# Optimization experiments

Hardware: AMD Instinct MI355X
Metric: run time of the kernel (lower is better)

Reference implementation:

```python
import jax, jax.numpy as jnp
import numpy as np

DIM = 2048
NUM_HEADS = 16
HEAD_DIM = DIM // NUM_HEADS
FF_MULT = 2
ROPE_BASE = 10000.0
EPS = 1e-6


def _rmsnorm(x, g):
    return x * jax.lax.rsqrt(jnp.mean(x * x, axis=-1, keepdims=True) + EPS) * g


def _rope_tables(seq_len):
    half = HEAD_DIM // 2
    inv_freq = 1.0 / (ROPE_BASE ** (2.0 * jnp.arange(half, dtype=jnp.float32) / HEAD_DIM))
    angles = jnp.arange(seq_len, dtype=jnp.float32)[:, None] * inv_freq[None, :]  # (S, half)
    return jnp.cos(angles), jnp.sin(angles)


def _apply_rope(x, cos, sin):
    # x: (B, H, S, D); cos/sin: (S, D/2). Interleaved pairs (RoFormer form).
    x_even = x[..., 0::2]
    x_odd = x[..., 1::2]
    c = cos[None, None].astype(x.dtype)
    s = sin[None, None].astype(x.dtype)
    rot_even = x_even * c - x_odd * s
    rot_odd = x_odd * c + x_even * s
    return jnp.stack([rot_even, rot_odd], axis=-1).reshape(x.shape)


def setup_inputs() -> dict:
    key = jax.random.key(0)
    ks = jax.random.split(key, 7)
    B, S = 2, 2048
    scale = 1.0 / np.sqrt(DIM)
    return {
        "x": jax.random.normal(ks[0], (B, S, DIM), dtype=jnp.float32),
        "w_qkv": jax.random.normal(ks[1], (DIM, 3 * DIM), dtype=jnp.float32) * scale,
        "w_out": jax.random.normal(ks[2], (DIM, DIM), dtype=jnp.float32) * scale,
        "w_fc": jax.random.normal(ks[3], (DIM, DIM * FF_MULT), dtype=jnp.float32) * scale,
        "w_proj": jax.random.normal(ks[4], (DIM * FF_MULT, DIM), dtype=jnp.float32) / np.sqrt(DIM * FF_MULT),
        "g_in": jnp.ones((DIM,), dtype=jnp.float32),
        "g_ff": jnp.ones((DIM,), dtype=jnp.float32),
    }


def reference(x, w_qkv, w_out, w_fc, w_proj, g_in, g_ff):
    B, S, D = x.shape
    # --- attention branch ---
    h = _rmsnorm(x, g_in)
    qkv = h @ w_qkv  # (B, S, 3D)
    q, k, v = jnp.split(qkv, 3, axis=-1)
    def heads(t):
        return t.reshape(B, S, NUM_HEADS, HEAD_DIM).transpose(0, 2, 1, 3)
    q, k, v = heads(q), heads(k), heads(v)  # (B, H, S, Dh)
    cos, sin = _rope_tables(S)
    q = _apply_rope(q, cos, sin)
    k = _apply_rope(k, cos, sin)
    scores = jnp.einsum("bhqd,bhkd->bhqk", q, k) / jnp.asarray(np.sqrt(HEAD_DIM), x.dtype)
    causal = jnp.tril(jnp.ones((S, S), dtype=bool))
    scores = jnp.where(causal[None, None], scores, jnp.asarray(-jnp.inf, scores.dtype))
    attn = jax.nn.softmax(scores, axis=-1)
    out = jnp.einsum("bhqk,bhkd->bhqd", attn, v)  # (B, H, S, Dh)
    out = out.transpose(0, 2, 1, 3).reshape(B, S, D)
    x = x + out @ w_out
    # --- feed-forward branch ---
    h = _rmsnorm(x, g_ff)
    x = x + jax.nn.gelu(h @ w_fc) @ w_proj
    return x


if __name__ == "__main__":
    inp = setup_inputs()
    y = reference(**inp)
    print(y.shape, y.dtype)
```

## Files before the change

kernel.cpp:

```cpp
#include <hip/hip_runtime.h>
#include <math.h>

typedef __bf16 bf16x8 __attribute__((ext_vector_type(8)));
typedef float  f32x4  __attribute__((ext_vector_type(4)));

#define DEV __device__ __forceinline__

DEV void gload16(const void* g, void* l) {
  __builtin_amdgcn_global_load_lds(
      (const __attribute__((address_space(1))) void*)g,
      (__attribute__((address_space(3))) void*)l, 16, 0, 0);
}

__global__ __launch_bounds__(256) void transpose_cvt(
    const float* __restrict__ in, __bf16* __restrict__ outT, int R, int C) {
  __shared__ float t[64][65];
  const int c0 = blockIdx.x * 64, r0 = blockIdx.y * 64;
  const int tid = threadIdx.x;
#pragma unroll
  for (int i = 0; i < 4; i++) {
    int r = (tid >> 4) + i * 16;
    int cf = tid & 15;
    float4 v = *(const float4*)(in + (size_t)(r0 + r) * C + c0 + cf * 4);
    t[r][cf * 4 + 0] = v.x; t[r][cf * 4 + 1] = v.y;
    t[r][cf * 4 + 2] = v.z; t[r][cf * 4 + 3] = v.w;
  }
  __syncthreads();
#pragma unroll
  for (int i = 0; i < 2; i++) {
    int c = (tid >> 3) + i * 32;
    int r8 = tid & 7;
    bf16x8 ov;
#pragma unroll
    for (int k = 0; k < 8; k++) ov[k] = (__bf16)t[r8 * 8 + k][c];
    *(bf16x8*)(outT + (size_t)(c0 + c) * R + r0 + r8 * 8) = ov;
  }
}

__global__ __launch_bounds__(256) void rmsnorm_kernel(
    const float* __restrict__ x, const float* __restrict__ g, __bf16* __restrict__ out) {
  const int r = blockIdx.x, t = threadIdx.x;
  const float4* xr = (const float4*)(x + (size_t)r * 2048);
  float4 a = xr[2 * t], b = xr[2 * t + 1];
  float ss = a.x * a.x + a.y * a.y + a.z * a.z + a.w * a.w +
             b.x * b.x + b.y * b.y + b.z * b.z + b.w * b.w;
#pragma unroll
  for (int mk = 1; mk < 64; mk <<= 1) ss += __shfl_xor(ss, mk);
  __shared__ float red[4];
  if ((t & 63) == 0) red[t >> 6] = ss;
  __syncthreads();
  const float sc = rsqrtf((red[0] + red[1] + red[2] + red[3]) * (1.0f / 2048.0f) + 1e-6f);
  const float4* gr = (const float4*)g;
  float4 ga = gr[2 * t], gb = gr[2 * t + 1];
  bf16x8 ov;
  ov[0] = (__bf16)(a.x * sc * ga.x); ov[1] = (__bf16)(a.y * sc * ga.y);
  ov[2] = (__bf16)(a.z * sc * ga.z); ov[3] = (__bf16)(a.w * sc * ga.w);
  ov[4] = (__bf16)(b.x * sc * gb.x); ov[5] = (__bf16)(b.y * sc * gb.y);
  ov[6] = (__bf16)(b.z * sc * gb.z); ov[7] = (__bf16)(b.w * sc * gb.w);
  *(bf16x8*)(out + (size_t)r * 2048 + t * 8) = ov;
}

template <int EPI>
__global__ __launch_bounds__(256) void gemm_bt(
    const __bf16* __restrict__ A, const __bf16* __restrict__ BT,
    void* __restrict__ Cout, const float* __restrict__ res, int M, int N, int K) {
  __shared__ char lds[32768];
  char* As = lds;
  char* Bs = lds + 16384;
  const int tid = threadIdx.x;
  const int lane = tid & 63;
  const int bn = blockIdx.x, bm = blockIdx.y;
  const int wm = tid >> 7, wn = (tid >> 6) & 1;

  f32x4 acc[4][4];
#pragma unroll
  for (int i = 0; i < 4; i++)
#pragma unroll
    for (int j = 0; j < 4; j++) acc[i][j] = (f32x4){0.f, 0.f, 0.f, 0.f};

  const size_t strideA = (size_t)K * 2;
  const char* ga[4];
  const char* gb[4];
#pragma unroll
  for (int t = 0; t < 4; t++) {
    int gg = t * 256 + tid;
    int row = gg >> 3, slot = gg & 7;
    ga[t] = (const char*)A + (size_t)(bm * 128 + row) * strideA + ((slot ^ (row & 7)) << 4);
    gb[t] = (const char*)BT + (size_t)(bn * 128 + row) * strideA + ((slot ^ (row & 7)) << 4);
  }

  for (int k0 = 0; k0 < K; k0 += 64) {
    __syncthreads();
#pragma unroll
    for (int t = 0; t < 4; t++) {
      int gg = t * 256 + tid;
      gload16(ga[t], As + gg * 16);
      gload16(gb[t], Bs + gg * 16);
      ga[t] += 128;
      gb[t] += 128;
    }
    __syncthreads();
#pragma unroll
    for (int kk = 0; kk < 2; kk++) {
      bf16x8 a[4], b[4];
      const int c16 = kk * 4 + (lane >> 4);
#pragma unroll
      for (int i = 0; i < 4; i++) {
        int ra = wm * 64 + i * 16 + (lane & 15);
        a[i] = *(const bf16x8*)(As + ra * 128 + ((c16 ^ (ra & 7)) << 4));
        int rb = wn * 64 + i * 16 + (lane & 15);
        b[i] = *(const bf16x8*)(Bs + rb * 128 + ((c16 ^ (rb & 7)) << 4));
      }
#pragma unroll
      for (int i = 0; i < 4; i++)
#pragma unroll
        for (int j = 0; j < 4; j++)
          acc[i][j] = __builtin_amdgcn_mfma_f32_16x16x32_bf16(a[i], b[j], acc[i][j], 0, 0, 0);
    }
  }

#pragma unroll
  for (int i = 0; i < 4; i++)
#pragma unroll
    for (int j = 0; j < 4; j++)
#pragma unroll
      for (int r = 0; r < 4; r++) {
        int row = bm * 128 + wm * 64 + i * 16 + ((lane >> 4) << 2) + r;
        int col = bn * 128 + wn * 64 + j * 16 + (lane & 15);
        size_t idx = (size_t)row * N + col;
        float v = acc[i][j][r];
        if (EPI == 0) {
          ((__bf16*)Cout)[idx] = (__bf16)v;
        } else if (EPI == 1) {
          ((float*)Cout)[idx] = v + res[idx];
        } else {
          float u = 0.7978845608028654f * (v + 0.044715f * v * v * v);
          ((__bf16*)Cout)[idx] = (__bf16)(0.5f * v * (1.0f + tanhf(u)));
        }
      }
}

#define MMQ(IB, JB, AR, BR)                                                   \
  __builtin_amdgcn_s_setprio(1);                                              \
  _Pragma("unroll") for (int i = 0; i < 4; i++)                               \
      _Pragma("unroll") for (int j = 0; j < 2; j++)                           \
          _Pragma("unroll") for (int kk = 0; kk < 2; kk++)                    \
              acc[(IB)*4 + i][(JB)*2 + j] =                                   \
      __builtin_amdgcn_mfma_f32_16x16x32_bf16(                                \
          AR[i][kk], BR[j][kk], acc[(IB)*4 + i][(JB)*2 + j], 0, 0, 0);        \
  __builtin_amdgcn_s_setprio(0);

template <int EPI>
__global__ __launch_bounds__(512, 2) void gemm256(
    const __bf16* __restrict__ A, const __bf16* __restrict__ BT,
    void* __restrict__ Cout, const float* __restrict__ res, int M, int N, int K) {
  __shared__ char lds[131072];
  const int tid = threadIdx.x, lane = tid & 63, w = tid >> 6;
  const int wm = w >> 2, wn = w & 3;
  const int bn = blockIdx.x, bm = blockIdx.y;

  f32x4 acc[8][4];
#pragma unroll
  for (int i = 0; i < 8; i++)
#pragma unroll
    for (int j = 0; j < 4; j++) acc[i][j] = (f32x4){0.f, 0.f, 0.f, 0.f};

  const size_t strideA = (size_t)K * 2;
  const int r0 = tid >> 3, s0 = tid & 7;
  const int r1 = r0 + 64;
  const char* Ab0 = (const char*)A + (size_t)(bm * 256) * strideA;
  const char* Bb0 = (const char*)BT + (size_t)(bn * 256) * strideA;

  auto stage = [&](int isB, int h, int kt, int buf) {
    const char* g = (isB ? Bb0 : Ab0) + (size_t)(h * 128) * strideA + (size_t)kt * 128;
    char* d = lds + isB * 65536 + buf * 32768 + h * 16384;
    gload16(g + (size_t)r0 * strideA + ((s0 ^ (r0 & 7)) << 4), d + tid * 16);
    gload16(g + (size_t)r1 * strideA + ((s0 ^ (r1 & 7)) << 4), d + (tid + 512) * 16);
  };
  auto ldA = [&](bf16x8 (&a)[4][2], int buf, int bank) {
    const char* base = lds + buf * 32768 + wm * 16384;
#pragma unroll
    for (int i = 0; i < 4; i++)
#pragma unroll
      for (int kk = 0; kk < 2; kk++) {
        int rl = bank * 64 + i * 16 + (lane & 15);
        int c16 = kk * 4 + (lane >> 4);
        a[i][kk] = *(const bf16x8*)(base + rl * 128 + ((c16 ^ (rl & 7)) << 4));
      }
  };
  auto ldB = [&](bf16x8 (&b)[2][2], int buf, int jb) {
    const char* base = lds + 65536 + buf * 32768 + (wn >> 1) * 16384;
#pragma unroll
    for (int j = 0; j < 2; j++)
#pragma unroll
      for (int kk = 0; kk < 2; kk++) {
        int rl = (wn & 1) * 64 + jb * 32 + j * 16 + (lane & 15);
        int c16 = kk * 4 + (lane >> 4);
        b[j][kk] = *(const bf16x8*)(base + rl * 128 + ((c16 ^ (rl & 7)) << 4));
      }
  };

  const int NT = K >> 6;
  stage(1, 0, 0, 0); stage(1, 1, 0, 0); stage(0, 0, 0, 0); stage(0, 1, 0, 0);
  stage(1, 0, 1, 1); stage(1, 1, 1, 1); stage(0, 0, 1, 1); stage(0, 1, 1, 1);
  asm volatile("s_waitcnt vmcnt(6)" ::: "memory");
  __builtin_amdgcn_s_barrier();

  bf16x8 a[4][2], b0[2][2], b1[2][2];
  for (int it = 0; it < (NT >> 1); ++it) {
    const int e = 2 * it;
    const int ep = (e + 2 < NT) ? e + 2 : NT - 1;
    const int op = (e + 3 < NT) ? e + 3 : NT - 1;
    ldA(a, 0, 0); ldB(b0, 0, 0);
    __builtin_amdgcn_s_barrier();
    MMQ(0, 0, a, b0);
    __builtin_amdgcn_s_barrier();
    ldB(b1, 0, 1);
    __builtin_amdgcn_s_barrier();
    MMQ(0, 1, a, b1);
    __builtin_amdgcn_s_barrier();
    ldA(a, 0, 1); stage(1, 0, ep, 0);
    __builtin_amdgcn_s_barrier();
    MMQ(1, 1, a, b1);
    __builtin_amdgcn_s_barrier();
    stage(1, 1, ep, 0);
    asm volatile("s_waitcnt vmcnt(4)" ::: "memory");
    __builtin_amdgcn_s_barrier();
    MMQ(1, 0, a, b0);
    __builtin_amdgcn_s_barrier();
    ldA(a, 1, 0); ldB(b0, 1, 0); stage(0, 0, ep, 0);
    __builtin_amdgcn_s_barrier();
    MMQ(0, 0, a, b0);
    __builtin_amdgcn_s_barrier();
    ldB(b1, 1, 1); stage(0, 1, ep, 0);
    __builtin_amdgcn_s_barrier();
    MMQ(0, 1, a, b1);
    __builtin_amdgcn_s_barrier();
    ldA(a, 1, 1); stage(1, 0, op, 1);
    __builtin_amdgcn_s_barrier();
    MMQ(1, 1, a, b1);
    __builtin_amdgcn_s_barrier();
    stage(1, 1, op, 1); stage(0, 0, op, 1); stage(0, 1, op, 1);
    asm volatile("s_waitcnt vmcnt(6)" ::: "memory");
    __builtin_amdgcn_s_barrier();
    MMQ(1, 0, a, b0);
    __builtin_amdgcn_s_barrier();
  }
  asm volatile("s_waitcnt vmcnt(0)" ::: "memory");

#pragma unroll
  for (int i = 0; i < 8; i++)
#pragma unroll
    for (int j = 0; j < 4; j++)
#pragma unroll
      for (int r = 0; r < 4; r++) {
        int row = bm * 256 + wm * 128 + i * 16 + ((lane >> 4) << 2) + r;
        int col = bn * 256 + wn * 64 + j * 16 + (lane & 15);
        size_t idx = (size_t)row * N + col;
        float v = acc[i][j][r];
        if (EPI == 0) {
          ((__bf16*)Cout)[idx] = (__bf16)v;
        } else if (EPI == 1) {
          ((float*)Cout)[idx] = v + res[idx];
        } else {
          float u = 0.7978845608028654f * (v + 0.044715f * v * v * v);
          ((__bf16*)Cout)[idx] = (__bf16)(0.5f * v * (1.0f + tanhf(u)));
        }
      }
}

__global__ __launch_bounds__(256) void rope_tables(float* __restrict__ tab) {
  const int idx = blockIdx.x * 256 + threadIdx.x;
  const int s = idx >> 6, j = idx & 63;
  const float inv = powf(10000.0f, -(float)j / 64.0f);
  const float a = (float)s * inv;
  tab[idx] = cosf(a);
  tab[131072 + idx] = sinf(a);
}

__global__ __launch_bounds__(256) void rope_apply(
    const __bf16* __restrict__ qkv, const float* __restrict__ tab,
    __bf16* __restrict__ qr, __bf16* __restrict__ kr) {
  const int idx = blockIdx.x * 256 + threadIdx.x;
  const int ch = idx & 15;
  const int h = (idx >> 4) & 15;
  const int s = (idx >> 8) & 2047;
  const int b = idx >> 19;
  const float4 c4 = *(const float4*)(tab + (s << 6) + ch * 4);
  const float4 s4 = *(const float4*)(tab + 131072 + (s << 6) + ch * 4);
  const float cc[4] = {c4.x, c4.y, c4.z, c4.w};
  const float ss[4] = {s4.x, s4.y, s4.z, s4.w};
  const size_t qi = ((size_t)(b * 2048 + s)) * 6144 + h * 128 + ch * 8;
  const size_t qo = ((size_t)((b * 16 + h) * 2048 + s)) * 128 + ch * 8;
  bf16x8 vq = *(const bf16x8*)(qkv + qi);
  bf16x8 vk = *(const bf16x8*)(qkv + qi + 2048);
  bf16x8 oq, ok;
#pragma unroll
  for (int p = 0; p < 4; p++) {
    float e = (float)vq[2 * p], o = (float)vq[2 * p + 1];
    oq[2 * p] = (__bf16)(e * cc[p] - o * ss[p]);
    oq[2 * p + 1] = (__bf16)(o * cc[p] + e * ss[p]);
    e = (float)vk[2 * p]; o = (float)vk[2 * p + 1];
    ok[2 * p] = (__bf16)(e * cc[p] - o * ss[p]);
    ok[2 * p + 1] = (__bf16)(o * cc[p] + e * ss[p]);
  }
  *(bf16x8*)(qr + qo) = oq;
  *(bf16x8*)(kr + qo) = ok;
}

__global__ __launch_bounds__(256) void v_transpose(
    const __bf16* __restrict__ qkv, __bf16* __restrict__ vt) {
  __shared__ __bf16 t[32][33];
  const int s0 = blockIdx.x * 32, d0 = blockIdx.y * 32, bh = blockIdx.z;
  const int b = bh >> 4, h = bh & 15;
  const int tx = threadIdx.x, ty = threadIdx.y;
#pragma unroll
  for (int i = 0; i < 4; i++)
    t[ty + 8 * i][tx] =
        qkv[((size_t)(b * 2048 + s0 + ty + 8 * i)) * 6144 + 4096 + h * 128 + d0 + tx];
  __syncthreads();
#pragma unroll
  for (int i = 0; i < 4; i++)
    vt[((size_t)bh * 128 + d0 + ty + 8 * i) * 2048 + s0 + tx] = t[tx][ty + 8 * i];
}

__global__ __launch_bounds__(512) void flash_attn(
    const __bf16* __restrict__ qg, const __bf16* __restrict__ kg,
    const __bf16* __restrict__ vtg, __bf16* __restrict__ og) {
  __shared__ char lds[81920];
  const int tid = threadIdx.x, lane = tid & 63, w = tid >> 6;
  const int h = blockIdx.y, b = blockIdx.z;
  const int bh = b * 16 + h;
  const __bf16* qb = qg + (size_t)bh * 2048 * 128;
  const char* kbb = (const char*)(kg + (size_t)bh * 2048 * 128);
  const char* vbb = (const char*)(vtg + (size_t)bh * 128 * 2048);
  char* Pw = lds + 65536 + w * 2048;

  const char* gK[2];
  const char* gV[2];
#pragma unroll
  for (int t = 0; t < 2; t++) {
    int gg = t * 512 + tid;
    int rk = gg >> 4, sk = gg & 15;
    gK[t] = kbb + rk * 256 + ((sk ^ (rk & 15)) << 4);
    int rv = gg >> 3, sv = gg & 7;
    gV[t] = vbb + rv * 4096 + ((sv ^ (rv & 7)) << 4);
  }

  const float SL2E = 0.08838834764831845f * 1.4426950408889634f;

  auto stageKV = [&](int kt, int buf) {
#pragma unroll
    for (int t = 0; t < 2; t++) {
      int gg = t * 512 + tid;
      gload16(gK[t] + (size_t)kt * 16384, lds + buf * 16384 + gg * 16);
      gload16(gV[t] + (size_t)kt * 128, lds + 32768 + buf * 16384 + gg * 16);
    }
  };

  auto run_qtile = [&](int qt) {
    const int qrow0 = qt * 128 + w * 16;
    bf16x8 qf[4];
#pragma unroll
    for (int c = 0; c < 4; c++) {
      bf16x8 raw = *(const bf16x8*)(qb + (size_t)(qrow0 + (lane & 15)) * 128 +
                                    c * 32 + ((lane >> 4) << 3));
#pragma unroll
      for (int e = 0; e < 8; e++) qf[c][e] = (__bf16)((float)raw[e] * SL2E);
    }
    float m[4], lsp[4];
    f32x4 o[8];
#pragma unroll
    for (int r = 0; r < 4; r++) { m[r] = -__builtin_inff(); lsp[r] = 0.f; }
#pragma unroll
    for (int n = 0; n < 8; n++) o[n] = (f32x4){0.f, 0.f, 0.f, 0.f};

    const int NKT = 2 * qt + 2;
    stageKV(0, 0);

    for (int kt = 0; kt < NKT; kt++) {
      const int cur = kt & 1;
      const char* Ks = lds + cur * 16384;
      const char* Vs = lds + 32768 + cur * 16384;
      if (kt < NKT - 1) {
        stageKV(kt + 1, cur ^ 1);
        asm volatile("s_waitcnt vmcnt(4)" ::: "memory");
      } else {
        asm volatile("s_waitcnt vmcnt(0)" ::: "memory");
      }
      __builtin_amdgcn_s_barrier();

      f32x4 s[4];
      __builtin_amdgcn_s_setprio(1);
#pragma unroll
      for (int n = 0; n < 4; n++) {
        s[n] = (f32x4){0.f, 0.f, 0.f, 0.f};
#pragma unroll
        for (int c = 0; c < 4; c++) {
          int krow = n * 16 + (lane & 15);
          int c16 = c * 4 + (lane >> 4);
          bf16x8 kf = *(const bf16x8*)(Ks + krow * 256 + ((c16 ^ (krow & 15)) << 4));
          s[n] = __builtin_amdgcn_mfma_f32_16x16x32_bf16(qf[c], kf, s[n], 0, 0, 0);
        }
      }
      __builtin_amdgcn_s_setprio(0);

      if (kt * 64 + 63 > qrow0) {
#pragma unroll
        for (int r = 0; r < 4; r++) {
          const int qrow = qrow0 + ((lane >> 4) << 2) + r;
#pragma unroll
          for (int n = 0; n < 4; n++) {
            int col = kt * 64 + n * 16 + (lane & 15);
            if (col > qrow) s[n][r] = -__builtin_inff();
          }
        }
      }

      float tmx[4];
#pragma unroll
      for (int r = 0; r < 4; r++)
        tmx[r] = fmaxf(fmaxf(s[0][r], s[1][r]), fmaxf(s[2][r], s[3][r]));
      bool hot = (tmx[0] > m[0] + 8.f) | (tmx[1] > m[1] + 8.f) |
                 (tmx[2] > m[2] + 8.f) | (tmx[3] > m[3] + 8.f);
      if (__any(hot)) {
        float fc[4];
#pragma unroll
        for (int r = 0; r < 4; r++) {
          float gmx = tmx[r];
#pragma unroll
          for (int mk = 1; mk < 16; mk <<= 1) gmx = fmaxf(gmx, __shfl_xor(gmx, mk));
          float nm = fmaxf(m[r], gmx);
          fc[r] = __builtin_amdgcn_exp2f(m[r] - nm);
          m[r] = nm;
          lsp[r] *= fc[r];
        }
#pragma unroll
        for (int n = 0; n < 8; n++) {
          o[n][0] *= fc[0]; o[n][1] *= fc[1]; o[n][2] *= fc[2]; o[n][3] *= fc[3];
        }
      }

      float p[4][4];
#pragma unroll
      for (int r = 0; r < 4; r++) {
        float sum = 0.f;
#pragma unroll
        for (int n = 0; n < 4; n++) {
          float pv = __builtin_amdgcn_exp2f(s[n][r] - m[r]);
          p[n][r] = pv;
          sum += pv;
        }
        lsp[r] += sum;
      }

#pragma unroll
      for (int n = 0; n < 4; n++)
#pragma unroll
        for (int r = 0; r < 4; r++) {
          int prow = ((lane >> 4) << 2) + r;
          int col = n * 16 + (lane & 15);
          int ch = col >> 3;
          *(__bf16*)(Pw + prow * 128 + ((ch ^ (prow & 7)) << 4) + ((col & 7) << 1)) =
              (__bf16)p[n][r];
        }

      __builtin_amdgcn_s_setprio(1);
#pragma unroll
      for (int kk = 0; kk < 2; kk++) {
        int prow = lane & 15;
        int pc = kk * 4 + (lane >> 4);
        bf16x8 pf = *(const bf16x8*)(Pw + prow * 128 + ((pc ^ (prow & 7)) << 4));
#pragma unroll
        for (int n = 0; n < 8; n++) {
          int vr = n * 16 + (lane & 15);
          bf16x8 vf = *(const bf16x8*)(Vs + vr * 128 + ((pc ^ (vr & 7)) << 4));
          o[n] = __builtin_amdgcn_mfma_f32_16x16x32_bf16(pf, vf, o[n], 0, 0, 0);
        }
      }
      __builtin_amdgcn_s_setprio(0);
      __builtin_amdgcn_s_barrier();
    }

    float inv[4];
#pragma unroll
    for (int r = 0; r < 4; r++) {
      float ls = lsp[r];
#pragma unroll
      for (int mk = 1; mk < 16; mk <<= 1) ls += __shfl_xor(ls, mk);
      inv[r] = 1.0f / ls;
    }
#pragma unroll
    for (int n = 0; n < 8; n++)
#pragma unroll
      for (int r = 0; r < 4; r++) {
        int qrow = qrow0 + ((lane >> 4) << 2) + r;
        og[(size_t)(b * 2048 + qrow) * 2048 + h * 128 + n * 16 + (lane & 15)] =
            (__bf16)(o[n][r] * inv[r]);
      }
  };

  run_qtile(15 - (int)blockIdx.x);
  run_qtile((int)blockIdx.x);
}

extern "C" void kernel_launch(void* const* d_in, const int* in_sizes, int n_in,
                              void* d_out, int out_size, void* d_ws, size_t ws_size,
                              hipStream_t stream) {
  const float* x = (const float*)d_in[0];
  const float* w_qkv = (const float*)d_in[1];
  const float* w_out = (const float*)d_in[2];
  const float* w_fc = (const float*)d_in[3];
  const float* w_proj = (const float*)d_in[4];
  const float* g_in = (const float*)d_in[5];
  const float* g_ff = (const float*)d_in[6];
  float* out = (float*)d_out;
  char* ws = (char*)d_ws;

  constexpr size_t O_WQKV = 0;
  constexpr size_t O_WOUT = 25165824;
  constexpr size_t O_WFC = 33554432;
  constexpr size_t O_WPROJ = 50331648;
  constexpr size_t O_H = 67108864;
  constexpr size_t O_QKV = 83886080;
  constexpr size_t O_Q = 134217728;
  constexpr size_t O_K = 150994944;
  constexpr size_t O_VT = 167772160;
  constexpr size_t O_TAB = 184549376;
  constexpr size_t O_ATTN = 185597952;
  constexpr size_t O_X1 = 202375168;

  __bf16* wqkvT = (__bf16*)(ws + O_WQKV);
  __bf16* woutT = (__bf16*)(ws + O_WOUT);
  __bf16* wfcT = (__bf16*)(ws + O_WFC);
  __bf16* wprojT = (__bf16*)(ws + O_WPROJ);
  __bf16* h = (__bf16*)(ws + O_H);
  __bf16* qkv = (__bf16*)(ws + O_QKV);
  __bf16* fcact = (__bf16*)(ws + O_QKV);
  __bf16* qr = (__bf16*)(ws + O_Q);
  __bf16* kr = (__bf16*)(ws + O_K);
  __bf16* vt = (__bf16*)(ws + O_VT);
  float* tab = (float*)(ws + O_TAB);
  __bf16* attn = (__bf16*)(ws + O_ATTN);
  float* x1 = (float*)(ws + O_X1);

  transpose_cvt<<<dim3(96, 32), 256, 0, stream>>>(w_qkv, wqkvT, 2048, 6144);
  transpose_cvt<<<dim3(32, 32), 256, 0, stream>>>(w_out, woutT, 2048, 2048);
  transpose_cvt<<<dim3(64, 32), 256, 0, stream>>>(w_fc, wfcT, 2048, 4096);
  transpose_cvt<<<dim3(32, 64), 256, 0, stream>>>(w_proj, wprojT, 4096, 2048);

  rmsnorm_kernel<<<4096, 256, 0, stream>>>(x, g_in, h);
  gemm_bt<0><<<dim3(48, 32), 256, 0, stream>>>(h, wqkvT, (void*)qkv, nullptr, 4096, 6144, 2048);
  rope_tables<<<512, 256, 0, stream>>>(tab);
  rope_apply<<<4096, 256, 0, stream>>>(qkv, tab, qr, kr);
  v_transpose<<<dim3(64, 4, 32), dim3(32, 8), 0, stream>>>(qkv, vt);
  flash_attn<<<dim3(8, 16, 2), 512, 0, stream>>>(qr, kr, vt, attn);
  gemm_bt<1><<<dim3(16, 32), 256, 0, stream>>>(attn, woutT, (void*)x1, x, 4096, 2048, 2048);
  rmsnorm_kernel<<<4096, 256, 0, stream>>>(x1, g_ff, h);
  gemm256<2><<<dim3(16, 16), 512, 0, stream>>>(h, wfcT, (void*)fcact, nullptr, 4096, 4096, 2048);
  gemm_bt<1><<<dim3(16, 32), 256, 0, stream>>>(fcact, wprojT, (void*)out, x1, 4096, 2048, 4096);
}
```

Baseline: 488.6 us.

## Fuse RoPE and V transpose into QKV GEMM epilogue

```diff
diff --git a/kernel.cpp b/kernel.cpp
--- a/kernel.cpp
+++ b/kernel.cpp
@@ -2,6 +2,7 @@
 #include <math.h>
 
 typedef __bf16 bf16x8 __attribute__((ext_vector_type(8)));
+typedef __bf16 bf16x4 __attribute__((ext_vector_type(4)));
 typedef float  f32x4  __attribute__((ext_vector_type(4)));
 
 #define DEV __device__ __forceinline__
@@ -140,6 +141,104 @@
       }
 }
 
+__global__ __launch_bounds__(256) void gemm_qkv(
+    const __bf16* __restrict__ A, const __bf16* __restrict__ BT,
+    const float2* __restrict__ tab, __bf16* __restrict__ qr,
+    __bf16* __restrict__ kr, __bf16* __restrict__ vt, int K) {
+  __shared__ char lds[32768];
+  char* As = lds;
+  char* Bs = lds + 16384;
+  const int tid = threadIdx.x;
+  const int lane = tid & 63;
+  const int bn = blockIdx.x, bm = blockIdx.y;
+  const int wm = tid >> 7, wn = (tid >> 6) & 1;
+
+  f32x4 acc[4][4];
+#pragma unroll
+  for (int i = 0; i < 4; i++)
+#pragma unroll
+    for (int j = 0; j < 4; j++) acc[i][j] = (f32x4){0.f, 0.f, 0.f, 0.f};
+
+  const size_t strideA = (size_t)K * 2;
+  const char* ga[4];
+  const char* gb[4];
+#pragma unroll
+  for (int t = 0; t < 4; t++) {
+    int gg = t * 256 + tid;
+    int row = gg >> 3, slot = gg & 7;
+    ga[t] = (const char*)A + (size_t)(bm * 128 + row) * strideA + ((slot ^ (row & 7)) << 4);
+    gb[t] = (const char*)BT + (size_t)(bn * 128 + row) * strideA + ((slot ^ (row & 7)) << 4);
+  }
+
+  for (int k0 = 0; k0 < K; k0 += 64) {
+    __syncthreads();
+#pragma unroll
+    for (int t = 0; t < 4; t++) {
+      int gg = t * 256 + tid;
+      gload16(ga[t], As + gg * 16);
+      gload16(gb[t], Bs + gg * 16);
+      ga[t] += 128;
+      gb[t] += 128;
+    }
+    __syncthreads();
+#pragma unroll
+    for (int kk = 0; kk < 2; kk++) {
+      bf16x8 a[4], b[4];
+      const int c16 = kk * 4 + (lane >> 4);
+#pragma unroll
+      for (int i = 0; i < 4; i++) {
+        int ra = wm * 64 + i * 16 + (lane & 15);
+        a[i] = *(const bf16x8*)(As + ra * 128 + ((c16 ^ (ra & 7)) << 4));
+        int rb = wn * 64 + i * 16 + (lane & 15);
+        b[i] = *(const bf16x8*)(Bs + rb * 128 + ((c16 ^ (rb & 7)) << 4));
+      }
+#pragma unroll
+      for (int i = 0; i < 4; i++)
+#pragma unroll
+        for (int j = 0; j < 4; j++)
+          acc[i][j] = __builtin_amdgcn_mfma_f32_16x16x32_bf16(a[i], b[j], acc[i][j], 0, 0, 0);
+    }
+  }
+
+  const int colbase = bn * 128 + wn * 64;
+  if (bn < 32) {
+#pragma unroll
+    for (int i = 0; i < 4; i++)
+#pragma unroll
+      for (int j = 0; j < 4; j++) {
+        int col = colbase + j * 16 + (lane & 15);
+        int isK = col >> 11;
+        int hh = (col >> 7) & 15, d = col & 127, jj = d >> 1;
+        __bf16* dst = isK ? kr : qr;
+#pragma unroll
+        for (int r = 0; r < 4; r++) {
+          int row = bm * 128 + wm * 64 + i * 16 + ((lane >> 4) << 2) + r;
+          int bb = row >> 11, srel = row & 2047;
+          float2 cs = tab[(srel << 6) + jj];
+          float me = acc[i][j][r];
+          float pv = __shfl_xor(me, 1);
+          float ov = (lane & 1) ? (me * cs.x + pv * cs.y)
+                                : (me * cs.x - pv * cs.y);
+          dst[((size_t)((bb * 16 + hh) * 2048 + srel)) * 128 + d] = (__bf16)ov;
+        }
+      }
+  } else {
+#pragma unroll
+    for (int i = 0; i < 4; i++)
+#pragma unroll
+      for (int j = 0; j < 4; j++) {
+        int col = colbase + j * 16 + (lane & 15) - 4096;
+        int hh = col >> 7, d = col & 127;
+        int row0 = bm * 128 + wm * 64 + i * 16 + ((lane >> 4) << 2);
+        int bb = row0 >> 11, srel = row0 & 2047;
+        bf16x4 pk;
+#pragma unroll
+        for (int r = 0; r < 4; r++) pk[r] = (__bf16)acc[i][j][r];
+        *(bf16x4*)(vt + ((size_t)((bb * 16 + hh) * 128 + d)) * 2048 + srel) = pk;
+      }
+  }
+}
+
 #define MMQ(IB, JB, AR, BR)                                                   \
   __builtin_amdgcn_s_setprio(1);                                              \
   _Pragma("unroll") for (int i = 0; i < 4; i++)                               \
@@ -269,59 +368,12 @@
       }
 }
 
-__global__ __launch_bounds__(256) void rope_tables(float* __restrict__ tab) {
+__global__ __launch_bounds__(256) void rope_tables(float2* __restrict__ tab) {
   const int idx = blockIdx.x * 256 + threadIdx.x;
   const int s = idx >> 6, j = idx & 63;
   const float inv = powf(10000.0f, -(float)j / 64.0f);
   const float a = (float)s * inv;
-  tab[idx] = cosf(a);
-  tab[131072 + idx] = sinf(a);
-}
-
-__global__ __launch_bounds__(256) void rope_apply(
-    const __bf16* __restrict__ qkv, const float* __restrict__ tab,
-    __bf16* __restrict__ qr, __bf16* __restrict__ kr) {
-  const int idx = blockIdx.x * 256 + threadIdx.x;
-  const int ch = idx & 15;
-  const int h = (idx >> 4) & 15;
-  const int s = (idx >> 8) & 2047;
-  const int b = idx >> 19;
-  const float4 c4 = *(const float4*)(tab + (s << 6) + ch * 4);
-  const float4 s4 = *(const float4*)(tab + 131072 + (s << 6) + ch * 4);
-  const float cc[4] = {c4.x, c4.y, c4.z, c4.w};
-  const float ss[4] = {s4.x, s4.y, s4.z, s4.w};
-  const size_t qi = ((size_t)(b * 2048 + s)) * 6144 + h * 128 + ch * 8;
-  const size_t qo = ((size_t)((b * 16 + h) * 2048 + s)) * 128 + ch * 8;
-  bf16x8 vq = *(const bf16x8*)(qkv + qi);
-  bf16x8 vk = *(const bf16x8*)(qkv + qi + 2048);
-  bf16x8 oq, ok;
-#pragma unroll
-  for (int p = 0; p < 4; p++) {
-    float e = (float)vq[2 * p], o = (float)vq[2 * p + 1];
-    oq[2 * p] = (__bf16)(e * cc[p] - o * ss[p]);
-    oq[2 * p + 1] = (__bf16)(o * cc[p] + e * ss[p]);
-    e = (float)vk[2 * p]; o = (float)vk[2 * p + 1];
-    ok[2 * p] = (__bf16)(e * cc[p] - o * ss[p]);
-    ok[2 * p + 1] = (__bf16)(o * cc[p] + e * ss[p]);
-  }
-  *(bf16x8*)(qr + qo) = oq;
-  *(bf16x8*)(kr + qo) = ok;
-}
-
-__global__ __launch_bounds__(256) void v_transpose(
-    const __bf16* __restrict__ qkv, __bf16* __restrict__ vt) {
-  __shared__ __bf16 t[32][33];
-  const int s0 = blockIdx.x * 32, d0 = blockIdx.y * 32, bh = blockIdx.z;
-  const int b = bh >> 4, h = bh & 15;
-  const int tx = threadIdx.x, ty = threadIdx.y;
-#pragma unroll
-  for (int i = 0; i < 4; i++)
-    t[ty + 8 * i][tx] =
-        qkv[((size_t)(b * 2048 + s0 + ty + 8 * i)) * 6144 + 4096 + h * 128 + d0 + tx];
-  __syncthreads();
-#pragma unroll
-  for (int i = 0; i < 4; i++)
-    vt[((size_t)bh * 128 + d0 + ty + 8 * i) * 2048 + s0 + tx] = t[tx][ty + 8 * i];
+  tab[idx] = make_float2(cosf(a), sinf(a));
 }
 
 __global__ __launch_bounds__(512) void flash_attn(
@@ -535,12 +587,11 @@
   __bf16* wfcT = (__bf16*)(ws + O_WFC);
   __bf16* wprojT = (__bf16*)(ws + O_WPROJ);
   __bf16* h = (__bf16*)(ws + O_H);
-  __bf16* qkv = (__bf16*)(ws + O_QKV);
   __bf16* fcact = (__bf16*)(ws + O_QKV);
   __bf16* qr = (__bf16*)(ws + O_Q);
   __bf16* kr = (__bf16*)(ws + O_K);
   __bf16* vt = (__bf16*)(ws + O_VT);
-  float* tab = (float*)(ws + O_TAB);
+  float2* tab = (float2*)(ws + O_TAB);
   __bf16* attn = (__bf16*)(ws + O_ATTN);
   float* x1 = (float*)(ws + O_X1);
 
@@ -549,11 +600,9 @@
   transpose_cvt<<<dim3(64, 32), 256, 0, stream>>>(w_fc, wfcT, 2048, 4096);
   transpose_cvt<<<dim3(32, 64), 256, 0, stream>>>(w_proj, wprojT, 4096, 2048);
 
+  rope_tables<<<512, 256, 0, stream>>>(tab);
   rmsnorm_kernel<<<4096, 256, 0, stream>>>(x, g_in, h);
-  gemm_bt<0><<<dim3(48, 32), 256, 0, stream>>>(h, wqkvT, (void*)qkv, nullptr, 4096, 6144, 2048);
-  rope_tables<<<512, 256, 0, stream>>>(tab);
-  rope_apply<<<4096, 256, 0, stream>>>(qkv, tab, qr, kr);
-  v_transpose<<<dim3(64, 4, 32), dim3(32, 8), 0, stream>>>(qkv, vt);
+  gemm_qkv<<<dim3(48, 32), 256, 0, stream>>>(h, wqkvT, tab, qr, kr, vt, 2048);
   flash_attn<<<dim3(8, 16, 2), 512, 0, stream>>>(qr, kr, vt, attn);
   gemm_bt<1><<<dim3(16, 32), 256, 0, stream>>>(attn, woutT, (void*)x1, x, 4096, 2048, 2048);
   rmsnorm_kernel<<<4096, 256, 0, stream>>>(x1, g_ff, h);
```

After: 459.9 us. 1.06x faster.
